# Optimization experiments

Measured on AMD Instinct MI355X. Metric: run time of the kernel, lower is better.

The kernel has to match this reference:

```python
import jax, jax.numpy as jnp
import numpy as np

HIDDEN = 2048
N_HEADS = 16
HEAD_DIM = HIDDEN // N_HEADS
INV_NORM = 1.0 / float(np.sqrt(HEAD_DIM))
BETA = 1.0


def setup_inputs() -> dict:
    key = jax.random.key(0)
    ks = jax.random.split(key, 12)
    B, S, H = 2, 2048, HIDDEN
    scale = 1.0 / float(np.sqrt(H))
    return {
        "hidden_states": jax.random.normal(ks[0], (B, S, H), jnp.float32),
        "residual": jax.random.normal(ks[1], (B, S, H), jnp.float32),
        "alibi": jax.random.normal(ks[2], (B * N_HEADS, 1, S), jnp.float32),
        "Wq": jax.random.normal(ks[3], (H, H), jnp.float32) * scale,
        "bq": jnp.zeros((H,), jnp.float32),
        "Wk": jax.random.normal(ks[4], (H, H), jnp.float32) * scale,
        "bk": jnp.zeros((H,), jnp.float32),
        "Wv": jax.random.normal(ks[5], (H, H), jnp.float32) * scale,
        "bv": jnp.zeros((H,), jnp.float32),
        "Wd": jax.random.normal(ks[6], (H, H), jnp.float32) * scale,
        "bd": jnp.zeros((H,), jnp.float32),
    }


def reference(hidden_states, residual, alibi, Wq, bq, Wk, bk, Wv, bv, Wd, bd):
    B, S, H = hidden_states.shape
    # separate QKV projections (nn.Linear: x @ W^T + b)
    q = hidden_states @ Wq.T + bq
    k = hidden_states @ Wk.T + bk
    v = hidden_states @ Wv.T + bv
    # [B, n_heads, S, head_dim]
    q = q.reshape(B, S, N_HEADS, HEAD_DIM).transpose(0, 2, 1, 3)
    k = k.reshape(B, S, N_HEADS, HEAD_DIM).transpose(0, 2, 1, 3)
    v = v.reshape(B, S, N_HEADS, HEAD_DIM).transpose(0, 2, 1, 3)
    # baddbmm: scores = beta * alibi + inv_norm * q @ k^T, per (batch*head)
    alibi_bh = alibi.reshape(B, N_HEADS, 1, S)  # broadcasts over query dim
    scores = BETA * alibi_bh + INV_NORM * jnp.einsum("bhqd,bhkd->bhqk", q, k)
    probs = jax.nn.softmax(scores.astype(jnp.float32), axis=-1).astype(v.dtype)
    # attention dropout: p=0.0 (identity)
    ctx = jnp.einsum("bhqk,bhkd->bhqd", probs, v)  # [B,H,S,D]
    ctx = ctx.transpose(0, 2, 1, 3).reshape(B, S, H)
    out = ctx @ Wd.T + bd
    # hidden dropout p=0.0 then residual add (dropout_add)
    return out + residual
```

## Files before the change

### kernel.cpp

```cpp
#include <hip/hip_runtime.h>

#define HID   2048
#define NHEAD 16
#define HD    128
#define SEQ   2048
#define BATCH 2
#define MROWS (BATCH*SEQ)
#define NQKV  (3*HID)
#define INV_NORM 0.08838834764831845f
#define LOG2E    1.4426950408889634f
#define SCALE_L2 (INV_NORM*LOG2E)

typedef __attribute__((ext_vector_type(8)))  __bf16 bf16x8;
typedef __attribute__((ext_vector_type(4)))  float  f32x4;
typedef __attribute__((ext_vector_type(16))) float  f32x16;

typedef __attribute__((address_space(1))) void GV;
typedef __attribute__((address_space(3))) void LV;

__device__ __forceinline__ void async16(const void* g, void* l) {
  __builtin_amdgcn_global_load_lds((const GV*)g, (LV*)l, 16, 0, 0);
}

__device__ __forceinline__ unsigned short f2bf(float f) {
  unsigned u = __builtin_bit_cast(unsigned, f);
  u += 0x7FFFu + ((u >> 16) & 1u);
  return (unsigned short)(u >> 16);
}

__device__ __forceinline__ unsigned pkbf(float a, float b) {
#if __has_builtin(__builtin_amdgcn_cvt_pk_bf16_f32)
  typedef __attribute__((ext_vector_type(2))) __bf16 bf16x2;
  bf16x2 r = __builtin_amdgcn_cvt_pk_bf16_f32(a, b);
  return __builtin_bit_cast(unsigned, r);
#else
  return (unsigned)f2bf(a) | ((unsigned)f2bf(b) << 16);
#endif
}

__device__ __forceinline__ void mfma16(f32x4& c, bf16x8 a, bf16x8 b) {
  c = __builtin_amdgcn_mfma_f32_16x16x32_bf16(a, b, c, 0, 0, 0);
}

__global__ __launch_bounds__(256) void cvt_kernel(const float* __restrict__ src,
                                                  unsigned short* __restrict__ dst, int n) {
  int i = (blockIdx.x * 256 + threadIdx.x) * 4;
  if (i >= n) return;
  float4 v = *(const float4*)(src + i);
  ushort4 o;
  o.x = f2bf(v.x); o.y = f2bf(v.y); o.z = f2bf(v.z); o.w = f2bf(v.w);
  *(ushort4*)(dst + i) = o;
}

__global__ __launch_bounds__(256) void cvtw_kernel(const float* __restrict__ W0,
                                                   const float* __restrict__ W1,
                                                   const float* __restrict__ W2,
                                                   const float* __restrict__ W3,
                                                   unsigned short* __restrict__ dst) {
  int sel = blockIdx.y;
  const float* src = (sel == 0) ? W0 : (sel == 1) ? W1 : (sel == 2) ? W2 : W3;
  unsigned short* d = dst + (size_t)sel * HID * HID;
  int i = (blockIdx.x * 256 + threadIdx.x) * 4;
  float4 v = *(const float4*)(src + i);
  ushort4 o;
  o.x = f2bf(v.x); o.y = f2bf(v.y); o.z = f2bf(v.z); o.w = f2bf(v.w);
  *(ushort4*)(d + i) = o;
}

__device__ __forceinline__ void gemm_core(const unsigned short* __restrict__ A,
                                          const unsigned short* __restrict__ Bm,
                                          int K, int m0, int n0,
                                          unsigned short* As, unsigned short* Bs,
                                          f32x4 (&acc)[4][4]) {
  const int tid  = threadIdx.x;
  const int w    = tid >> 6;
  const int lane = tid & 63;
  const int l16  = lane & 15;
  const int quad = lane >> 4;
  const int wm   = (w & 1) * 64;
  const int wn   = (w >> 1) * 64;

  const f32x4 zero = {0.f, 0.f, 0.f, 0.f};
#pragma unroll
  for (int i = 0; i < 4; ++i)
#pragma unroll
    for (int j = 0; j < 4; ++j) acc[i][j] = zero;

  for (int k0 = 0; k0 < K; k0 += 64) {
    __syncthreads();
#pragma unroll
    for (int i = 0; i < 4; ++i) {
      int slot = i * 256 + w * 64 + lane;
      int r = slot >> 3;
      int c = (slot & 7) ^ (r & 7);
      async16(A  + (size_t)(m0 + r) * K + k0 + c * 8, (char*)As + (size_t)(i * 256 + w * 64) * 16);
      async16(Bm + (size_t)(n0 + r) * K + k0 + c * 8, (char*)Bs + (size_t)(i * 256 + w * 64) * 16);
    }
    __syncthreads();

#pragma unroll
    for (int kk = 0; kk < 2; ++kk) {
      bf16x8 af[4], bfp[4];
#pragma unroll
      for (int i = 0; i < 4; ++i) {
        int rr = wm + i * 16 + l16;
        af[i] = *(const bf16x8*)(As + ((rr * 8 + (((kk * 4 + quad)) ^ (rr & 7))) * 8));
      }
#pragma unroll
      for (int j = 0; j < 4; ++j) {
        int rr = wn + j * 16 + l16;
        bfp[j] = *(const bf16x8*)(Bs + ((rr * 8 + (((kk * 4 + quad)) ^ (rr & 7))) * 8));
      }
#pragma unroll
      for (int i = 0; i < 4; ++i)
#pragma unroll
        for (int j = 0; j < 4; ++j) mfma16(acc[i][j], af[i], bfp[j]);
    }
  }
}

__global__ __launch_bounds__(256) void gemm_qkv_kernel(
    const unsigned short* __restrict__ Xb, const unsigned short* __restrict__ Wb,
    const float* __restrict__ bq, const float* __restrict__ bk,
    const float* __restrict__ bv, unsigned short* __restrict__ Cout) {
  __shared__ __align__(16) unsigned short As[128 * 64];
  __shared__ __align__(16) unsigned short Bs[128 * 64];
  f32x4 acc[4][4];
  const int m0 = blockIdx.y * 128, n0 = blockIdx.x * 128;
  gemm_core(Xb, Wb, HID, m0, n0, As, Bs, acc);

  const int tid = threadIdx.x, w = tid >> 6, lane = tid & 63;
  const int l16 = lane & 15, quad = lane >> 4;
  const int wm = (w & 1) * 64, wn = (w >> 1) * 64;
#pragma unroll
  for (int j = 0; j < 4; ++j) {
    int ng = n0 + wn + j * 16 + l16;
    float bias = (ng < HID) ? bq[ng] : (ng < 2 * HID ? bk[ng - HID] : bv[ng - 2 * HID]);
#pragma unroll
    for (int i = 0; i < 4; ++i)
#pragma unroll
      for (int r = 0; r < 4; ++r) {
        int mg = m0 + wm + i * 16 + quad * 4 + r;
        Cout[(size_t)mg * NQKV + ng] = f2bf(acc[i][j][r] + bias);
      }
  }
}

__global__ __launch_bounds__(256) void gemm_out_kernel(
    const unsigned short* __restrict__ Ctx, const unsigned short* __restrict__ Wdb,
    const float* __restrict__ bd, const float* __restrict__ Res,
    float* __restrict__ Out) {
  __shared__ __align__(16) unsigned short As[128 * 64];
  __shared__ __align__(16) unsigned short Bs[128 * 64];
  f32x4 acc[4][4];
  const int m0 = blockIdx.y * 128, n0 = blockIdx.x * 128;
  gemm_core(Ctx, Wdb, HID, m0, n0, As, Bs, acc);

  const int tid = threadIdx.x, w = tid >> 6, lane = tid & 63;
  const int l16 = lane & 15, quad = lane >> 4;
  const int wm = (w & 1) * 64, wn = (w >> 1) * 64;
#pragma unroll
  for (int j = 0; j < 4; ++j) {
    int ng = n0 + wn + j * 16 + l16;
    float bias = bd[ng];
#pragma unroll
    for (int i = 0; i < 4; ++i)
#pragma unroll
      for (int r = 0; r < 4; ++r) {
        int mg = m0 + wm + i * 16 + quad * 4 + r;
        size_t off = (size_t)mg * HID + ng;
        Out[off] = acc[i][j][r] + bias + Res[off];
      }
  }
}

__global__ __launch_bounds__(256) void vtrans_kernel(const unsigned short* __restrict__ QKV,
                                                     unsigned short* __restrict__ Vt) {
  __shared__ __align__(16) unsigned short T[64][72];
  const int s0 = blockIdx.x * 64, d0 = blockIdx.y * 64, bh = blockIdx.z;
  const int b = bh >> 4, h = bh & 15;
  const int tid = threadIdx.x;
#pragma unroll
  for (int i = 0; i < 2; ++i) {
    int idx = i * 256 + tid;
    int r = idx >> 3, ch = idx & 7;
    const unsigned short* g = QKV + ((size_t)b * SEQ + s0 + r) * NQKV + 2 * HID + h * HD + d0 + ch * 8;
    *(uint4*)(&T[r][ch * 8]) = *(const uint4*)g;
  }
  __syncthreads();
#pragma unroll
  for (int i = 0; i < 2; ++i) {
    int idx = i * 256 + tid;
    int d = idx >> 3, ch = idx & 7;
    unsigned short v[8];
#pragma unroll
    for (int x = 0; x < 8; ++x) v[x] = T[ch * 8 + x][d];
    unsigned short* g = Vt + ((size_t)bh * HD + d0 + d) * SEQ + s0 + ch * 8;
    *(uint4*)g = *(const uint4*)v;
  }
}

__global__ __launch_bounds__(256, 2) void attn_kernel(
    const unsigned short* __restrict__ QKV, const unsigned short* __restrict__ Vt,
    const float* __restrict__ alibi, unsigned short* __restrict__ Ctx) {
  __shared__ __align__(16) char smem[51200];
  unsigned short* Ks  = (unsigned short*)smem;
  unsigned short* Vts = (unsigned short*)(smem + 16384);
  unsigned short* Ps  = (unsigned short*)(smem + 32768);
  unsigned short* Qs  = (unsigned short*)smem;

  const int tid = threadIdx.x, w = tid >> 6, lane = tid & 63;
  const int l32 = lane & 31, h = lane >> 5;
  const int q0 = blockIdx.x * 128;
  const int bh = blockIdx.y, b = bh >> 4, hh = bh & 15;
  const size_t rowbase = (size_t)b * SEQ;
  const float* ali = alibi + (size_t)bh * SEQ;
  const unsigned short* Vbh = Vt + (size_t)bh * HD * SEQ;

  {
    const unsigned short* qbase = QKV + (rowbase + q0) * NQKV + hh * HD;
#pragma unroll
    for (int i = 0; i < 8; ++i) {
      int slot = i * 256 + w * 64 + lane;
      int r = slot >> 4, c = (slot & 15) ^ (r & 15);
      async16(qbase + (size_t)r * NQKV + c * 8, (char*)Qs + (size_t)(i * 256 + w * 64) * 16);
    }
  }
  __syncthreads();
  bf16x8 qf[8];
  {
    int qr = w * 32 + l32;
#pragma unroll
    for (int ks = 0; ks < 8; ++ks) {
      int c = (ks * 2 + h) ^ (qr & 15);
      qf[ks] = *(const bf16x8*)(Qs + (qr * 16 + c) * 8);
    }
  }

  f32x16 oacc[4];
  float l_acc = 0.f;
#pragma unroll
  for (int nb = 0; nb < 4; ++nb)
#pragma unroll
    for (int r = 0; r < 16; ++r) oacc[nb][r] = 0.f;

  __syncthreads();

  for (int kt = 0; kt < SEQ / 64; ++kt) {
    {
      const unsigned short* kbase = QKV + (rowbase + kt * 64) * NQKV + HID + hh * HD;
#pragma unroll
      for (int i = 0; i < 4; ++i) {
        int slot = i * 256 + w * 64 + lane;
        int r = slot >> 4, c = (slot & 15) ^ (r & 15);
        async16(kbase + (size_t)r * NQKV + c * 8, (char*)Ks + (size_t)(i * 256 + w * 64) * 16);
      }
      const unsigned short* vbase = Vbh + kt * 64;
#pragma unroll
      for (int i = 0; i < 4; ++i) {
        int slot = i * 256 + w * 64 + lane;
        int r = slot >> 3, c = (slot & 7) ^ (r & 7);
        async16(vbase + (size_t)r * SEQ + c * 8, (char*)Vts + (size_t)(i * 256 + w * 64) * 16);
      }
    }
    __syncthreads();

    f32x16 sacc[2];
#pragma unroll
    for (int mb = 0; mb < 2; ++mb)
#pragma unroll
      for (int r = 0; r < 16; ++r) sacc[mb][r] = 0.f;
#pragma unroll
    for (int ks = 0; ks < 8; ++ks) {
      int c = (ks * 2 + h) ^ (l32 & 15);
#pragma unroll
      for (int mb = 0; mb < 2; ++mb) {
        bf16x8 kf = *(const bf16x8*)(Ks + ((mb * 32 + l32) * 16 + ((ks * 2 + h) ^ (l32 & 15))) * 8);
        sacc[mb] = __builtin_amdgcn_mfma_f32_32x32x16_bf16(kf, qf[ks], sacc[mb], 0, 0, 0);
      }
      (void)c;
    }

    const float* alik = ali + kt * 64 + 4 * h;
    const int qrow = w * 32 + l32;
#pragma unroll
    for (int mb = 0; mb < 2; ++mb) {
#pragma unroll
      for (int g = 0; g < 4; ++g) {
        float4 av = *(const float4*)(alik + mb * 32 + g * 8);
        float p0 = __builtin_amdgcn_exp2f(sacc[mb][g * 4 + 0] * SCALE_L2 + av.x * LOG2E);
        float p1 = __builtin_amdgcn_exp2f(sacc[mb][g * 4 + 1] * SCALE_L2 + av.y * LOG2E);
        float p2 = __builtin_amdgcn_exp2f(sacc[mb][g * 4 + 2] * SCALE_L2 + av.z * LOG2E);
        float p3 = __builtin_amdgcn_exp2f(sacc[mb][g * 4 + 3] * SCALE_L2 + av.w * LOG2E);
        l_acc += (p0 + p1) + (p2 + p3);
        uint2 pk;
        pk.x = pkbf(p0, p1);
        pk.y = pkbf(p2, p3);
        *(uint2*)(Ps + qrow * 72 + mb * 32 + g * 8 + 4 * h) = pk;
      }
    }

#pragma unroll
    for (int ks2 = 0; ks2 < 4; ++ks2) {
      bf16x8 pf = *(const bf16x8*)(Ps + qrow * 72 + ks2 * 16 + h * 8);
#pragma unroll
      for (int nb = 0; nb < 4; ++nb) {
        bf16x8 vf = *(const bf16x8*)(Vts + ((nb * 32 + l32) * 8 + ((ks2 * 2 + h) ^ (l32 & 7))) * 8);
        oacc[nb] = __builtin_amdgcn_mfma_f32_32x32x16_bf16(pf, vf, oacc[nb], 0, 0, 0);
      }
    }
    __syncthreads();
  }

  float lf = l_acc + __shfl_xor(l_acc, 32, 64);
  float rinv[16];
#pragma unroll
  for (int reg = 0; reg < 16; ++reg) {
    int row = (reg & 3) + 8 * (reg >> 2) + 4 * h;
    rinv[reg] = 1.0f / __shfl(lf, row, 64);
  }

#pragma unroll
  for (int nb = 0; nb < 4; ++nb)
#pragma unroll
    for (int reg = 0; reg < 16; ++reg) {
      int row = (reg & 3) + 8 * (reg >> 2) + 4 * h;
      size_t qg = rowbase + q0 + w * 32 + row;
      Ctx[qg * HID + hh * HD + nb * 32 + l32] = f2bf(oacc[nb][reg] * rinv[reg]);
    }
}

extern "C" void kernel_launch(void* const* d_in, const int* in_sizes, int n_in,
                              void* d_out, int out_size, void* d_ws, size_t ws_size,
                              hipStream_t stream) {
  const float* hidden   = (const float*)d_in[0];
  const float* residual = (const float*)d_in[1];
  const float* alibi    = (const float*)d_in[2];
  const float* Wq = (const float*)d_in[3];
  const float* bq = (const float*)d_in[4];
  const float* Wk = (const float*)d_in[5];
  const float* bk = (const float*)d_in[6];
  const float* Wv = (const float*)d_in[7];
  const float* bv = (const float*)d_in[8];
  const float* Wd = (const float*)d_in[9];
  const float* bd = (const float*)d_in[10];
  float* out = (float*)d_out;

  unsigned short* Xb    = (unsigned short*)d_ws;
  unsigned short* Wqkvb = Xb + (size_t)MROWS * HID;
  unsigned short* Wdb   = Wqkvb + (size_t)NQKV * HID;
  unsigned short* QKVb  = Wdb + (size_t)HID * HID;
  unsigned short* Ctxb  = QKVb + (size_t)MROWS * NQKV;
  unsigned short* Vtb   = Wqkvb;

  const int nX = MROWS * HID, nW = HID * HID;
  cvt_kernel<<<nX / 4 / 256, 256, 0, stream>>>(hidden, Xb, nX);
  cvtw_kernel<<<dim3(nW / 4 / 256, 4), 256, 0, stream>>>(Wq, Wk, Wv, Wd, Wqkvb);

  gemm_qkv_kernel<<<dim3(NQKV / 128, MROWS / 128), 256, 0, stream>>>(Xb, Wqkvb, bq, bk, bv, QKVb);
  vtrans_kernel<<<dim3(SEQ / 64, HD / 64, BATCH * NHEAD), 256, 0, stream>>>(QKVb, Vtb);
  attn_kernel<<<dim3(SEQ / 128, BATCH * NHEAD), 256, 0, stream>>>(QKVb, Vtb, alibi, Ctxb);
  gemm_out_kernel<<<dim3(HID / 128, MROWS / 128), 256, 0, stream>>>(Ctxb, Wdb, bd, residual, out);
}
```

Before: 440.9 us.

## Fuse V transpose into QKV GEMM epilogue and merge conversion kernels

The QKV GEMM epilogue now writes Q and K to a compact QK buffer and, for the V column tiles, transposes the tile through shared memory to write V^T directly. This removes the separate vtrans kernel, along with its extra global read and write of V. The two fp32-to-bf16 conversion kernels are merged into one launch. The fused epilogue adds two shared-memory barriers per V tile and reuses the GEMM's LDS for the transpose.

```diff
diff --git a/kernel.cpp b/kernel.cpp
--- a/kernel.cpp
+++ b/kernel.cpp
@@ -7,6 +7,7 @@
 #define BATCH 2
 #define MROWS (BATCH*SEQ)
 #define NQKV  (3*HID)
+#define NQK   (2*HID)
 #define INV_NORM 0.08838834764831845f
 #define LOG2E    1.4426950408889634f
 #define SCALE_L2 (INV_NORM*LOG2E)
@@ -42,29 +43,26 @@
   c = __builtin_amdgcn_mfma_f32_16x16x32_bf16(a, b, c, 0, 0, 0);
 }
 
-__global__ __launch_bounds__(256) void cvt_kernel(const float* __restrict__ src,
-                                                  unsigned short* __restrict__ dst, int n) {
-  int i = (blockIdx.x * 256 + threadIdx.x) * 4;
-  if (i >= n) return;
-  float4 v = *(const float4*)(src + i);
+#define NX4 2097152
+#define NW4 1048576
+__global__ __launch_bounds__(256) void cvt_all_kernel(
+    const float* __restrict__ X,  const float* __restrict__ W0,
+    const float* __restrict__ W1, const float* __restrict__ W2,
+    const float* __restrict__ W3, unsigned short* __restrict__ dst) {
+  long c = (long)blockIdx.x * 256 + threadIdx.x;
+  const float* src;
+  long off;
+  if (c < NX4) { src = X; off = c; }
+  else {
+    long r = c - NX4;
+    int t = (int)(r >> 20);
+    off = r & (NW4 - 1);
+    src = (t == 0) ? W0 : (t == 1) ? W1 : (t == 2) ? W2 : W3;
+  }
+  float4 v = ((const float4*)src)[off];
   ushort4 o;
   o.x = f2bf(v.x); o.y = f2bf(v.y); o.z = f2bf(v.z); o.w = f2bf(v.w);
-  *(ushort4*)(dst + i) = o;
-}
-
-__global__ __launch_bounds__(256) void cvtw_kernel(const float* __restrict__ W0,
-                                                   const float* __restrict__ W1,
-                                                   const float* __restrict__ W2,
-                                                   const float* __restrict__ W3,
-                                                   unsigned short* __restrict__ dst) {
-  int sel = blockIdx.y;
-  const float* src = (sel == 0) ? W0 : (sel == 1) ? W1 : (sel == 2) ? W2 : W3;
-  unsigned short* d = dst + (size_t)sel * HID * HID;
-  int i = (blockIdx.x * 256 + threadIdx.x) * 4;
-  float4 v = *(const float4*)(src + i);
-  ushort4 o;
-  o.x = f2bf(v.x); o.y = f2bf(v.y); o.z = f2bf(v.z); o.w = f2bf(v.w);
-  *(ushort4*)(d + i) = o;
+  ((ushort4*)dst)[c] = o;
 }
 
 __device__ __forceinline__ void gemm_core(const unsigned short* __restrict__ A,
@@ -122,9 +120,13 @@
 __global__ __launch_bounds__(256) void gemm_qkv_kernel(
     const unsigned short* __restrict__ Xb, const unsigned short* __restrict__ Wb,
     const float* __restrict__ bq, const float* __restrict__ bk,
-    const float* __restrict__ bv, unsigned short* __restrict__ Cout) {
-  __shared__ __align__(16) unsigned short As[128 * 64];
-  __shared__ __align__(16) unsigned short Bs[128 * 64];
+    const float* __restrict__ bv, unsigned short* __restrict__ QK,
+    unsigned short* __restrict__ Vt) {
+  __shared__ __align__(16) char smem[32768];
+  unsigned short* As = (unsigned short*)smem;
+  unsigned short* Bs = (unsigned short*)(smem + 16384);
+  unsigned short* T  = (unsigned short*)smem;
+
   f32x4 acc[4][4];
   const int m0 = blockIdx.y * 128, n0 = blockIdx.x * 128;
   gemm_core(Xb, Wb, HID, m0, n0, As, Bs, acc);
@@ -132,6 +134,8 @@
   const int tid = threadIdx.x, w = tid >> 6, lane = tid & 63;
   const int l16 = lane & 15, quad = lane >> 4;
   const int wm = (w & 1) * 64, wn = (w >> 1) * 64;
+
+  unsigned short cv[4][4][4];
 #pragma unroll
   for (int j = 0; j < 4; ++j) {
     int ng = n0 + wn + j * 16 + l16;
@@ -139,10 +143,51 @@
 #pragma unroll
     for (int i = 0; i < 4; ++i)
 #pragma unroll
-      for (int r = 0; r < 4; ++r) {
-        int mg = m0 + wm + i * 16 + quad * 4 + r;
-        Cout[(size_t)mg * NQKV + ng] = f2bf(acc[i][j][r] + bias);
-      }
+      for (int r = 0; r < 4; ++r) cv[i][j][r] = f2bf(acc[i][j][r] + bias);
+  }
+
+  if (n0 < 2 * HID) {
+#pragma unroll
+    for (int j = 0; j < 4; ++j) {
+      int ng = n0 + wn + j * 16 + l16;
+#pragma unroll
+      for (int i = 0; i < 4; ++i)
+#pragma unroll
+        for (int r = 0; r < 4; ++r) {
+          int mg = m0 + wm + i * 16 + quad * 4 + r;
+          QK[(size_t)mg * NQK + ng] = cv[i][j][r];
+        }
+    }
+  } else {
+    const int hh = (n0 - 2 * HID) >> 7;
+    const int b2 = m0 >> 11;
+    const int s0l = m0 & 2047;
+    unsigned short* Vdst = Vt + ((size_t)(b2 * NHEAD + hh) * HD) * SEQ;
+#pragma unroll
+    for (int p = 0; p < 2; ++p) {
+      __syncthreads();
+      if ((w >> 1) == p) {
+#pragma unroll
+        for (int j = 0; j < 4; ++j) {
+          int cl = j * 16 + l16;
+#pragma unroll
+          for (int i = 0; i < 4; ++i) {
+            ushort4 pk4;
+            pk4.x = cv[i][j][0]; pk4.y = cv[i][j][1];
+            pk4.z = cv[i][j][2]; pk4.w = cv[i][j][3];
+            *(ushort4*)(T + cl * 136 + wm + i * 16 + quad * 4) = pk4;
+          }
+        }
+      }
+      __syncthreads();
+#pragma unroll
+      for (int ii = 0; ii < 4; ++ii) {
+        int slot = ii * 256 + tid;
+        int d = slot >> 4, ch = slot & 15;
+        uint4 val = *(const uint4*)(T + d * 136 + ch * 8);
+        *(uint4*)(Vdst + (size_t)(p * 64 + d) * SEQ + s0l + ch * 8) = val;
+      }
+    }
   }
 }
 
@@ -150,8 +195,9 @@
     const unsigned short* __restrict__ Ctx, const unsigned short* __restrict__ Wdb,
     const float* __restrict__ bd, const float* __restrict__ Res,
     float* __restrict__ Out) {
-  __shared__ __align__(16) unsigned short As[128 * 64];
-  __shared__ __align__(16) unsigned short Bs[128 * 64];
+  __shared__ __align__(16) char smem[32768];
+  unsigned short* As = (unsigned short*)smem;
+  unsigned short* Bs = (unsigned short*)(smem + 16384);
   f32x4 acc[4][4];
   const int m0 = blockIdx.y * 128, n0 = blockIdx.x * 128;
   gemm_core(Ctx, Wdb, HID, m0, n0, As, Bs, acc);
@@ -174,34 +220,8 @@
   }
 }
 
-__global__ __launch_bounds__(256) void vtrans_kernel(const unsigned short* __restrict__ QKV,
-                                                     unsigned short* __restrict__ Vt) {
-  __shared__ __align__(16) unsigned short T[64][72];
-  const int s0 = blockIdx.x * 64, d0 = blockIdx.y * 64, bh = blockIdx.z;
-  const int b = bh >> 4, h = bh & 15;
-  const int tid = threadIdx.x;
-#pragma unroll
-  for (int i = 0; i < 2; ++i) {
-    int idx = i * 256 + tid;
-    int r = idx >> 3, ch = idx & 7;
-    const unsigned short* g = QKV + ((size_t)b * SEQ + s0 + r) * NQKV + 2 * HID + h * HD + d0 + ch * 8;
-    *(uint4*)(&T[r][ch * 8]) = *(const uint4*)g;
-  }
-  __syncthreads();
-#pragma unroll
-  for (int i = 0; i < 2; ++i) {
-    int idx = i * 256 + tid;
-    int d = idx >> 3, ch = idx & 7;
-    unsigned short v[8];
-#pragma unroll
-    for (int x = 0; x < 8; ++x) v[x] = T[ch * 8 + x][d];
-    unsigned short* g = Vt + ((size_t)bh * HD + d0 + d) * SEQ + s0 + ch * 8;
-    *(uint4*)g = *(const uint4*)v;
-  }
-}
-
 __global__ __launch_bounds__(256, 2) void attn_kernel(
-    const unsigned short* __restrict__ QKV, const unsigned short* __restrict__ Vt,
+    const unsigned short* __restrict__ QK, const unsigned short* __restrict__ Vt,
     const float* __restrict__ alibi, unsigned short* __restrict__ Ctx) {
   __shared__ __align__(16) char smem[51200];
   unsigned short* Ks  = (unsigned short*)smem;
@@ -218,12 +238,12 @@
   const unsigned short* Vbh = Vt + (size_t)bh * HD * SEQ;
 
   {
-    const unsigned short* qbase = QKV + (rowbase + q0) * NQKV + hh * HD;
+    const unsigned short* qbase = QK + (rowbase + q0) * NQK + hh * HD;
 #pragma unroll
     for (int i = 0; i < 8; ++i) {
       int slot = i * 256 + w * 64 + lane;
       int r = slot >> 4, c = (slot & 15) ^ (r & 15);
-      async16(qbase + (size_t)r * NQKV + c * 8, (char*)Qs + (size_t)(i * 256 + w * 64) * 16);
+      async16(qbase + (size_t)r * NQK + c * 8, (char*)Qs + (size_t)(i * 256 + w * 64) * 16);
     }
   }
   __syncthreads();
@@ -248,12 +268,12 @@
 
   for (int kt = 0; kt < SEQ / 64; ++kt) {
     {
-      const unsigned short* kbase = QKV + (rowbase + kt * 64) * NQKV + HID + hh * HD;
+      const unsigned short* kbase = QK + (rowbase + kt * 64) * NQK + HID + hh * HD;
 #pragma unroll
       for (int i = 0; i < 4; ++i) {
         int slot = i * 256 + w * 64 + lane;
         int r = slot >> 4, c = (slot & 15) ^ (r & 15);
-        async16(kbase + (size_t)r * NQKV + c * 8, (char*)Ks + (size_t)(i * 256 + w * 64) * 16);
+        async16(kbase + (size_t)r * NQK + c * 8, (char*)Ks + (size_t)(i * 256 + w * 64) * 16);
       }
       const unsigned short* vbase = Vbh + kt * 64;
 #pragma unroll
@@ -272,13 +292,11 @@
       for (int r = 0; r < 16; ++r) sacc[mb][r] = 0.f;
 #pragma unroll
     for (int ks = 0; ks < 8; ++ks) {
-      int c = (ks * 2 + h) ^ (l32 & 15);
 #pragma unroll
       for (int mb = 0; mb < 2; ++mb) {
         bf16x8 kf = *(const bf16x8*)(Ks + ((mb * 32 + l32) * 16 + ((ks * 2 + h) ^ (l32 & 15))) * 8);
         sacc[mb] = __builtin_amdgcn_mfma_f32_32x32x16_bf16(kf, qf[ks], sacc[mb], 0, 0, 0);
       }
-      (void)c;
     }
 
     const float* alik = ali + kt * 64 + 4 * h;
@@ -349,16 +367,13 @@
   unsigned short* Xb    = (unsigned short*)d_ws;
   unsigned short* Wqkvb = Xb + (size_t)MROWS * HID;
   unsigned short* Wdb   = Wqkvb + (size_t)NQKV * HID;
-  unsigned short* QKVb  = Wdb + (size_t)HID * HID;
-  unsigned short* Ctxb  = QKVb + (size_t)MROWS * NQKV;
-  unsigned short* Vtb   = Wqkvb;
-
-  const int nX = MROWS * HID, nW = HID * HID;
-  cvt_kernel<<<nX / 4 / 256, 256, 0, stream>>>(hidden, Xb, nX);
-  cvtw_kernel<<<dim3(nW / 4 / 256, 4), 256, 0, stream>>>(Wq, Wk, Wv, Wd, Wqkvb);
-
-  gemm_qkv_kernel<<<dim3(NQKV / 128, MROWS / 128), 256, 0, stream>>>(Xb, Wqkvb, bq, bk, bv, QKVb);
-  vtrans_kernel<<<dim3(SEQ / 64, HD / 64, BATCH * NHEAD), 256, 0, stream>>>(QKVb, Vtb);
-  attn_kernel<<<dim3(SEQ / 128, BATCH * NHEAD), 256, 0, stream>>>(QKVb, Vtb, alibi, Ctxb);
+  unsigned short* QKb   = Wdb + (size_t)HID * HID;
+  unsigned short* Vtb   = QKb + (size_t)MROWS * NQK;
+  unsigned short* Ctxb  = Vtb + (size_t)BATCH * NHEAD * HD * SEQ;
+
+  cvt_all_kernel<<<(NX4 + 4 * NW4) / 256, 256, 0, stream>>>(hidden, Wq, Wk, Wv, Wd, Xb);
+
+  gemm_qkv_kernel<<<dim3(NQKV / 128, MROWS / 128), 256, 0, stream>>>(Xb, Wqkvb, bq, bk, bv, QKb, Vtb);
+  attn_kernel<<<dim3(SEQ / 128, BATCH * NHEAD), 256, 0, stream>>>(QKb, Vtb, alibi, Ctxb);
   gemm_out_kernel<<<dim3(HID / 128, MROWS / 128), 256, 0, stream>>>(Ctxb, Wdb, bd, residual, out);
 }
```

Measured after the change: 454.1 us. 1.03x slower.
